# Kernel tuning notes

Measured on AMD Instinct MI355X. Metric: run time of the kernel, lower is better.

The kernel has to match this reference:

```python
import jax, jax.numpy as jnp
import numpy as np
from jax import lax

N_BOXES = 4000
NUM_CLASSES = 81  # class 0 is background, skipped like the torch loop


def _iou_matrix(boxes):
    # boxes: [N,4] as (x1,y1,x2,y2). Returns [N,N] pairwise IoU.
    x1, y1, x2, y2 = boxes[:, 0], boxes[:, 1], boxes[:, 2], boxes[:, 3]
    area = (x2 - x1) * (y2 - y1)
    ix1 = jnp.maximum(x1[:, None], x1[None, :])
    iy1 = jnp.maximum(y1[:, None], y1[None, :])
    ix2 = jnp.minimum(x2[:, None], x2[None, :])
    iy2 = jnp.minimum(y2[:, None], y2[None, :])
    inter = jnp.clip(ix2 - ix1, 0.0) * jnp.clip(iy2 - iy1, 0.0)
    return inter / (area[:, None] + area[None, :] - inter + 1e-9)


def _nms_keep(iou, score, valid, nms_thresh):
    # Greedy NMS in descending-score order, fixed shape. iou: [N,N].
    n = score.shape[0]
    order = jnp.argsort(-score)
    idx_range = jnp.arange(n)

    def body(i, keep):
        idx = order[i]
        cur = keep[idx]  # still alive -> it suppresses overlapping boxes
        row = iou[idx]
        sup = cur & (row > nms_thresh) & (idx_range != idx)
        return keep & ~sup

    keep = lax.fori_loop(0, n, body, valid)
    return keep & valid


def reference(bboxes, scores, conf_thresh, nms_thresh, max_instances):
    n = bboxes.shape[0]
    iou = _iou_matrix(bboxes)                       # [N,N], shared across classes
    scores_fg = scores[:, 1:].T                     # [C-1, N]
    valid = scores_fg > conf_thresh                 # per-class conf filter
    keep = jax.vmap(lambda s, v: _nms_keep(iou, s, v, nms_thresh))(scores_fg, valid)
    # Kept detections get their score; everything else -1 (padding sentinel).
    final = jnp.where(keep, scores_fg, -1.0)        # [C-1, N]
    top_vals, top_idx = lax.top_k(final.reshape(-1), max_instances)
    cls = top_idx // n                              # label = class_index - 1 (0-based fg)
    box_idx = top_idx % n
    preds = jnp.concatenate([bboxes[box_idx], top_vals[:, None]], axis=1)  # [K,5]
    valid_out = top_vals > 0.0
    preds = jnp.where(valid_out[:, None], preds, 0.0)
    labels = jnp.where(valid_out, cls, -1)
    return preds, labels


def setup_inputs() -> dict:
    key = jax.random.key(0)
    k1, k2, k3 = jax.random.split(key, 3)
    cxcy = jax.random.uniform(k1, (N_BOXES, 2), dtype=jnp.float32) * 1000.0
    wh = jax.random.uniform(k2, (N_BOXES, 2), dtype=jnp.float32) * 100.0 + 1.0
    bboxes = jnp.concatenate([cxcy - wh * 0.5, cxcy + wh * 0.5], axis=1)
    scores = jax.random.uniform(k3, (N_BOXES, NUM_CLASSES), dtype=jnp.float32)
    return {
        "bboxes": bboxes,
        "scores": scores,
        "conf_thresh": jnp.float32(0.5),
        "nms_thresh": jnp.float32(0.5),
        "max_instances": 100,
    }
```

## Files before the change

### kernel.cpp

```cpp
#include <hip/hip_runtime.h>
#include <stdint.h>

typedef unsigned long long u64;
typedef unsigned int u32;

#define NB    4000
#define NBP   4096
#define NCLS  80
#define ROWW  64
#define MAXI  100
#define NKEY  (NCLS * MAXI)
#define SMAX  4096
#define SELT  448
#define NTH   512

__device__ __forceinline__ u32 mono_f32(float f) {
    u32 u = __float_as_uint(f);
    return (u & 0x80000000u) ? ~u : (u | 0x80000000u);
}

__device__ __forceinline__ void find_cross(const u32* hist, int T, int lane,
                                           int* outB, int* outA) {
    int running = 0, B = -1, A = 0;
    for (int g = 0; g < 16 && B < 0; ++g) {
        const int d = 1023 - (g * 64 + lane);
        const int cnt = (int)hist[d];
        int pre = cnt;
        #pragma unroll
        for (int off = 1; off < 64; off <<= 1) {
            const int v = __shfl_up(pre, off);
            if (lane >= off) pre += v;
        }
        const int incl = running + pre;
        const int excl = incl - cnt;
        const u64 hm = __ballot(excl < T && incl >= T);
        if (hm != 0ull) {
            const int hl = (int)__builtin_ctzll(hm);
            B = __shfl(d, hl);
            A = __shfl(excl, hl);
        }
        running = __shfl(incl, 63);
    }
    *outB = B; *outA = A;
}

__global__ __launch_bounds__(256) void k_pre(const float4* __restrict__ boxes,
                                             const float* __restrict__ scores,
                                             const float* __restrict__ conf_t,
                                             const float* __restrict__ nms_t,
                                             u64* __restrict__ suppr,
                                             u64* __restrict__ pkeys) {
    const int tid = threadIdx.x;
    if (blockIdx.x < NB / 4) {
        const int i0  = blockIdx.x * 4;
        const float t = *nms_t;
        float4 bi[4]; float ai[4];
        #pragma unroll
        for (int r = 0; r < 4; ++r) {
            bi[r] = boxes[i0 + r];
            ai[r] = (bi[r].z - bi[r].x) * (bi[r].w - bi[r].y);
        }
        #pragma unroll
        for (int ch = 0; ch < 16; ++ch) {
            const int j = ch * 256 + tid;
            const bool inb = (j < NB);
            float4 bj = make_float4(0.f, 0.f, 0.f, 0.f);
            float aj = 0.f;
            if (inb) { bj = boxes[j]; aj = (bj.z - bj.x) * (bj.w - bj.y); }
            #pragma unroll
            for (int r = 0; r < 4; ++r) {
                bool bit = false;
                if (inb && j != i0 + r) {
                    const float ix1 = fmaxf(bi[r].x, bj.x), iy1 = fmaxf(bi[r].y, bj.y);
                    const float ix2 = fminf(bi[r].z, bj.z), iy2 = fminf(bi[r].w, bj.w);
                    const float inter = fmaxf(ix2 - ix1, 0.0f) * fmaxf(iy2 - iy1, 0.0f);
                    bit = inter / (ai[r] + aj - inter + 1e-9f) > t;
                }
                const u64 m = __ballot(bit);
                if ((tid & 63) == 0) suppr[(size_t)(i0 + r) * ROWW + (j >> 6)] = m;
            }
        }
    } else {
        const int idx = blockIdx.x - NB / 4;
        const int c   = idx >> 4;
        const int b   = ((idx & 15) << 8) | tid;
        const float conf = *conf_t;
        u64 key = 0;
        if (b < NB) {
            const float s = scores[b * 81 + c + 1];
            if (s > conf)
                key = ((u64)mono_f32(s) << 32) | (u64)(0xFFFFFFFFu - (u32)b);
        }
        pkeys[c * NBP + b] = key;
    }
}

__global__ __launch_bounds__(NTH) void k_classnms(const u64* __restrict__ pkeys,
                                                  const u64* __restrict__ suppr,
                                                  u64* __restrict__ cand) {
    __shared__ u64 skey[SMAX];
    __shared__ unsigned short sbox[SMAX];
    __shared__ int wsum[8];
    __shared__ int sh_kept, sh_M, sh_B, sh_A, sh_B2, sh_nvalid;

    u32* hist = (u32*)sbox;

    const int c    = blockIdx.x;
    const int tid  = threadIdx.x;
    const int lane = tid & 63;
    const int wid  = tid >> 6;

    u64 own[8];
    int cnt = 0;
    #pragma unroll
    for (int q = 0; q < 8; ++q) {
        own[q] = pkeys[c * NBP + tid + q * NTH];
        cnt += (own[q] != 0ull);
    }
    #pragma unroll
    for (int off = 1; off < 64; off <<= 1) cnt += __shfl_xor(cnt, off);
    if (lane == 0) wsum[wid] = cnt;
    __syncthreads();
    if (tid == 0) {
        int t = 0;
        #pragma unroll
        for (int w = 0; w < 8; ++w) t += wsum[w];
        sh_nvalid = t;
    }
    __syncthreads();
    const int nvalid = sh_nvalid;

    bool full = (nvalid <= 512);
    int kept = 0;

    for (int attempt = 0; attempt < 2; ++attempt) {
        int M;
        if (!full) {
            for (int i = tid; i < 1024; i += NTH) hist[i] = 0;
            if (tid == 0) sh_M = 0;
            __syncthreads();
            #pragma unroll
            for (int q = 0; q < 8; ++q)
                if (own[q] != 0ull)
                    atomicAdd(&hist[(u32)(own[q] >> 54) & 1023u], 1u);
            __syncthreads();
            if (tid < 64) {
                int B, A;
                find_cross(hist, SELT, lane, &B, &A);
                if (lane == 0) { sh_B = B; sh_A = A; }
            }
            __syncthreads();
            const int B = sh_B, A = sh_A;
            for (int i = tid; i < 1024; i += NTH) hist[i] = 0;
            __syncthreads();
            #pragma unroll
            for (int q = 0; q < 8; ++q)
                if (own[q] != 0ull && ((u32)(own[q] >> 54) & 1023u) == (u32)B)
                    atomicAdd(&hist[(u32)(own[q] >> 44) & 1023u], 1u);
            __syncthreads();
            if (tid < 64) {
                int B2, A2;
                find_cross(hist, SELT - A, lane, &B2, &A2);
                if (lane == 0) sh_B2 = B2;
            }
            __syncthreads();
            const int B2 = sh_B2;
            #pragma unroll
            for (int q = 0; q < 8; ++q) {
                bool sel = false;
                if (own[q] != 0ull) {
                    const int d = (int)((u32)(own[q] >> 54) & 1023u);
                    sel = (d > B) ||
                          (d == B && (int)((u32)(own[q] >> 44) & 1023u) >= B2);
                }
                const u64 bm = __ballot(sel);
                int wbase = 0;
                if (lane == 0 && bm) wbase = atomicAdd(&sh_M, (int)__popcll(bm));
                wbase = __shfl(wbase, 0);
                if (sel)
                    skey[wbase + (int)__popcll(bm & ((1ull << lane) - 1ull))] = own[q];
            }
            __syncthreads();
            M = sh_M;
        } else {
            if (tid == 0) sh_M = 0;
            __syncthreads();
            #pragma unroll
            for (int q = 0; q < 8; ++q) {
                const bool sel = (own[q] != 0ull);
                const u64 bm = __ballot(sel);
                int wbase = 0;
                if (lane == 0 && bm) wbase = atomicAdd(&sh_M, (int)__popcll(bm));
                wbase = __shfl(wbase, 0);
                if (sel)
                    skey[wbase + (int)__popcll(bm & ((1ull << lane) - 1ull))] = own[q];
            }
            __syncthreads();
            M = sh_M;
        }

        int S = 64;
        while (S < M) S <<= 1;
        for (int i = M + tid; i < S; i += NTH) skey[i] = 0;
        __syncthreads();

        for (int k2 = 2; k2 <= S; k2 <<= 1) {
            for (int j = k2 >> 1; j >= 64; j >>= 1) {
                for (int p = tid; p < (S >> 1); p += NTH) {
                    const int i0 = ((p & ~(j - 1)) << 1) | (p & (j - 1));
                    const u64 a = skey[i0], b = skey[i0 | j];
                    const bool up = ((i0 & k2) == 0);
                    if (up ? (a < b) : (a > b)) { skey[i0] = b; skey[i0 | j] = a; }
                }
                __syncthreads();
            }
            for (int base = 0; base < S; base += NTH) {
                const int i = base + tid;
                if (i < S) {
                    u64 x = skey[i];
                    #pragma unroll
                    for (int j2 = 32; j2 >= 1; j2 >>= 1) {
                        if (j2 < k2) {
                            const u64 y = __shfl_xor(x, j2);
                            const bool wantmax = (((i & k2) == 0) == ((i & j2) == 0));
                            x = wantmax ? (x > y ? x : y) : (x < y ? x : y);
                        }
                    }
                    skey[i] = x;
                }
            }
            __syncthreads();
        }

        for (int i = tid; i < S; i += NTH)
            sbox[i] = (unsigned short)(0xFFFFFFFFu - (u32)skey[i]);
        __syncthreads();

        if (tid < 64) {
            u64 keptmask = 0;
            int kp = 0;
            if (M > 0) {
                const int last = M - 1;
                u64 wA[16], wB[16];
                #pragma unroll
                for (int q = 0; q < 16; ++q) {
                    const int idx = (q <= last) ? q : last;
                    wA[q] = suppr[(size_t)sbox[idx] * ROWW + lane];
                }
                for (int cs = 0; cs < M && kp < MAXI; cs += 32) {
                    #pragma unroll
                    for (int q = 0; q < 16; ++q) {
                        const int want = cs + 16 + q;
                        const int idx = (want <= last) ? want : last;
                        wB[q] = suppr[(size_t)sbox[idx] * ROWW + lane];
                    }
                    #pragma unroll
                    for (int q = 0; q < 16; ++q) {
                        const int p = cs + q;
                        if (p < M && kp < MAXI) {
                            const bool sup = (__ballot((wA[q] & keptmask) != 0ull) != 0ull);
                            if (!sup) {
                                const int b = sbox[p];
                                if (lane == (b >> 6)) keptmask |= (1ull << (b & 63));
                                if (lane == 0) {
                                    const u32 mono = (u32)(skey[p] >> 32);
                                    const u32 flat = (u32)(c * NB + b);
                                    cand[c * MAXI + kp] =
                                        ((u64)mono << 32) | (u64)(0xFFFFFFFFu - flat);
                                }
                                kp++;
                            }
                        }
                    }
                    #pragma unroll
                    for (int q = 0; q < 16; ++q) {
                        const int want = cs + 32 + q;
                        const int idx = (want <= last) ? want : last;
                        wA[q] = suppr[(size_t)sbox[idx] * ROWW + lane];
                    }
                    #pragma unroll
                    for (int q = 0; q < 16; ++q) {
                        const int p = cs + 16 + q;
                        if (p < M && kp < MAXI) {
                            const bool sup = (__ballot((wB[q] & keptmask) != 0ull) != 0ull);
                            if (!sup) {
                                const int b = sbox[p];
                                if (lane == (b >> 6)) keptmask |= (1ull << (b & 63));
                                if (lane == 0) {
                                    const u32 mono = (u32)(skey[p] >> 32);
                                    const u32 flat = (u32)(c * NB + b);
                                    cand[c * MAXI + kp] =
                                        ((u64)mono << 32) | (u64)(0xFFFFFFFFu - flat);
                                }
                                kp++;
                            }
                        }
                    }
                }
            }
            if (lane == 0) sh_kept = kp;
        }
        __syncthreads();
        kept = sh_kept;

        if (kept >= MAXI || full) break;
        full = true;
    }

    for (int s = tid; s < MAXI; s += NTH)
        if (s >= kept) cand[c * MAXI + s] = 0;
}

__global__ __launch_bounds__(1024) void k_final(const u64* __restrict__ cand,
                                                const float4* __restrict__ boxes,
                                                float* __restrict__ out) {
    __shared__ u32 hist[1024];
    __shared__ u64 sel[256];
    __shared__ int wsum[16];
    __shared__ int sh_total, sh_A, sh_B, sh_bits, sh_M, sh_cnt;
    __shared__ u64 sh_prefix;

    const int tid  = threadIdx.x;
    const int lane = tid & 63;
    const int wid  = tid >> 6;

    u64 myk[8];
    int cnt = 0;
    #pragma unroll
    for (int q = 0; q < 8; ++q) {
        const int i = tid + (q << 10);
        myk[q] = (i < NKEY) ? cand[i] : 0ull;
        cnt += (myk[q] != 0ull);
    }
    #pragma unroll
    for (int off = 1; off < 64; off <<= 1) cnt += __shfl_xor(cnt, off);
    if (lane == 0) wsum[wid] = cnt;
    if (tid < 256) sel[tid] = 0;
    __syncthreads();
    if (tid == 0) {
        int t = 0;
        #pragma unroll
        for (int w = 0; w < 16; ++w) t += wsum[w];
        sh_total = t; sh_A = 0; sh_bits = 0; sh_prefix = 0; sh_cnt = 0;
    }
    __syncthreads();
    const int total = sh_total;
    const int Tt = (total < MAXI) ? total : MAXI;

    if (total > 0) {
        for (int lvl = 0; lvl < 6; ++lvl) {
            hist[tid & 1023] = 0;
            __syncthreads();
            const int bits = sh_bits;
            const u64 pref = sh_prefix;
            const int shift = 54 - bits;
            #pragma unroll
            for (int q = 0; q < 8; ++q) {
                const u64 k = myk[q];
                if (k != 0ull && (bits == 0 || (k >> (64 - bits)) == pref))
                    atomicAdd(&hist[(u32)(k >> shift) & 1023u], 1u);
            }
            __syncthreads();
            if (tid < 64) {
                const int T = Tt - sh_A;
                int B, A;
                find_cross(hist, T, lane, &B, &A);
                if (lane == 0) { sh_B = B; sh_A += A; }
            }
            __syncthreads();
            if (tid == 0) {
                sh_M = sh_A + (int)hist[sh_B];
                sh_prefix = (sh_prefix << 10) | (u32)sh_B;
                sh_bits += 10;
            }
            __syncthreads();
            if (sh_M <= 256) break;
        }
        const int bits = sh_bits;
        const u64 pref = sh_prefix;
        #pragma unroll
        for (int q = 0; q < 8; ++q) {
            const u64 k = myk[q];
            const bool s = (k != 0ull) && ((k >> (64 - bits)) >= pref);
            const u64 bm = __ballot(s);
            int wbase = 0;
            if (lane == 0 && bm) wbase = atomicAdd(&sh_cnt, (int)__popcll(bm));
            wbase = __shfl(wbase, 0);
            if (s) sel[wbase + (int)__popcll(bm & ((1ull << lane) - 1ull))] = k;
        }
    }

    if (tid < MAXI) {
        out[tid*5+0] = 0.0f; out[tid*5+1] = 0.0f; out[tid*5+2] = 0.0f;
        out[tid*5+3] = 0.0f; out[tid*5+4] = 0.0f;
        out[500 + tid] = -1.0f;
    }
    __syncthreads();
    if (tid < 256) {
        const u64 my = sel[tid];
        if (my != 0ull) {
            int r = 0;
            for (int j = 0; j < 256; ++j) r += (sel[j] > my);
            if (r < MAXI) {
                const u32 mono = (u32)(my >> 32);
                const float sc = __uint_as_float(mono ^ 0x80000000u);
                const u32 flat = 0xFFFFFFFFu - (u32)my;
                const int b    = (int)(flat % NB);
                const float4 bb = boxes[b];
                out[r*5+0] = bb.x; out[r*5+1] = bb.y;
                out[r*5+2] = bb.z; out[r*5+3] = bb.w;
                out[r*5+4] = sc;
                out[500 + r] = (float)(flat / NB);
            }
        }
    }
}

extern "C" void kernel_launch(void* const* d_in, const int* in_sizes, int n_in,
                              void* d_out, int out_size, void* d_ws, size_t ws_size,
                              hipStream_t stream) {
    const float4* bboxes = (const float4*)d_in[0];
    const float*  scores = (const float*)d_in[1];
    const float*  conf_t = (const float*)d_in[2];
    const float*  nms_t  = (const float*)d_in[3];

    char* ws = (char*)d_ws;
    u64* suppr = (u64*)ws;
    u64* pkeys = (u64*)(ws + 2048000);
    u64* cand  = (u64*)(ws + 2048000 + 2621440);

    k_pre<<<NB / 4 + 16 * NCLS, 256, 0, stream>>>(bboxes, scores, conf_t, nms_t,
                                                  suppr, pkeys);
    k_classnms<<<NCLS, NTH, 0, stream>>>(pkeys, suppr, cand);
    k_final<<<1, 1024, 0, stream>>>(cand, bboxes, (float*)d_out);
}
```

Before: 124.3 us.

## Replace precomputed IoU bitmask with on-the-fly IoU against kept boxes

Removes the kernel that built the full 4000x4000 suppression bitmask and the per-class key buffer. Each class block now builds its keys from scores directly and copies all boxes into shared memory. During the greedy scan it tests each candidate's IoU only against the at most 100 boxes already kept, held two per lane, instead of reading bitmask rows from global memory. This drops a launch and about 2 MB of global traffic, but the candidate loop becomes serial with a per-candidate division and shared-memory read and no prefetch batching.

```diff
diff --git a/kernel.cpp b/kernel.cpp
--- a/kernel.cpp
+++ b/kernel.cpp
@@ -5,9 +5,7 @@
 typedef unsigned int u32;
 
 #define NB    4000
-#define NBP   4096
 #define NCLS  80
-#define ROWW  64
 #define MAXI  100
 #define NKEY  (NCLS * MAXI)
 #define SMAX  4096
@@ -44,88 +42,49 @@
     *outB = B; *outA = A;
 }
 
-__global__ __launch_bounds__(256) void k_pre(const float4* __restrict__ boxes,
+__global__ __launch_bounds__(NTH) void k_nms(const float4* __restrict__ boxes,
                                              const float* __restrict__ scores,
                                              const float* __restrict__ conf_t,
                                              const float* __restrict__ nms_t,
-                                             u64* __restrict__ suppr,
-                                             u64* __restrict__ pkeys) {
-    const int tid = threadIdx.x;
-    if (blockIdx.x < NB / 4) {
-        const int i0  = blockIdx.x * 4;
-        const float t = *nms_t;
-        float4 bi[4]; float ai[4];
-        #pragma unroll
-        for (int r = 0; r < 4; ++r) {
-            bi[r] = boxes[i0 + r];
-            ai[r] = (bi[r].z - bi[r].x) * (bi[r].w - bi[r].y);
-        }
-        #pragma unroll
-        for (int ch = 0; ch < 16; ++ch) {
-            const int j = ch * 256 + tid;
-            const bool inb = (j < NB);
-            float4 bj = make_float4(0.f, 0.f, 0.f, 0.f);
-            float aj = 0.f;
-            if (inb) { bj = boxes[j]; aj = (bj.z - bj.x) * (bj.w - bj.y); }
-            #pragma unroll
-            for (int r = 0; r < 4; ++r) {
-                bool bit = false;
-                if (inb && j != i0 + r) {
-                    const float ix1 = fmaxf(bi[r].x, bj.x), iy1 = fmaxf(bi[r].y, bj.y);
-                    const float ix2 = fminf(bi[r].z, bj.z), iy2 = fminf(bi[r].w, bj.w);
-                    const float inter = fmaxf(ix2 - ix1, 0.0f) * fmaxf(iy2 - iy1, 0.0f);
-                    bit = inter / (ai[r] + aj - inter + 1e-9f) > t;
-                }
-                const u64 m = __ballot(bit);
-                if ((tid & 63) == 0) suppr[(size_t)(i0 + r) * ROWW + (j >> 6)] = m;
-            }
-        }
-    } else {
-        const int idx = blockIdx.x - NB / 4;
-        const int c   = idx >> 4;
-        const int b   = ((idx & 15) << 8) | tid;
-        const float conf = *conf_t;
-        u64 key = 0;
-        if (b < NB) {
-            const float s = scores[b * 81 + c + 1];
-            if (s > conf)
-                key = ((u64)mono_f32(s) << 32) | (u64)(0xFFFFFFFFu - (u32)b);
-        }
-        pkeys[c * NBP + b] = key;
-    }
-}
-
-__global__ __launch_bounds__(NTH) void k_classnms(const u64* __restrict__ pkeys,
-                                                  const u64* __restrict__ suppr,
-                                                  u64* __restrict__ cand) {
+                                             u64* __restrict__ cand) {
     __shared__ u64 skey[SMAX];
-    __shared__ unsigned short sbox[SMAX];
+    __shared__ float4 sboxes[NB];
+    __shared__ u32 hist[1024];
     __shared__ int wsum[8];
     __shared__ int sh_kept, sh_M, sh_B, sh_A, sh_B2, sh_nvalid;
-
-    u32* hist = (u32*)sbox;
 
     const int c    = blockIdx.x;
     const int tid  = threadIdx.x;
     const int lane = tid & 63;
     const int wid  = tid >> 6;
+    const float conf = *conf_t;
+    const float t    = *nms_t;
+
+    for (int i = tid; i < NB; i += NTH) sboxes[i] = boxes[i];
 
     u64 own[8];
     int cnt = 0;
     #pragma unroll
     for (int q = 0; q < 8; ++q) {
-        own[q] = pkeys[c * NBP + tid + q * NTH];
-        cnt += (own[q] != 0ull);
+        const int b = tid + q * NTH;
+        u64 k = 0;
+        if (b < NB) {
+            const float s = scores[b * 81 + c + 1];
+            if (s > conf)
+                k = ((u64)mono_f32(s) << 32) | (u64)(0xFFFFFFFFu - (u32)b);
+        }
+        own[q] = k;
+        cnt += (k != 0ull);
     }
     #pragma unroll
     for (int off = 1; off < 64; off <<= 1) cnt += __shfl_xor(cnt, off);
     if (lane == 0) wsum[wid] = cnt;
     __syncthreads();
     if (tid == 0) {
-        int t = 0;
+        int tt = 0;
         #pragma unroll
-        for (int w = 0; w < 8; ++w) t += wsum[w];
-        sh_nvalid = t;
+        for (int w = 0; w < 8; ++w) tt += wsum[w];
+        sh_nvalid = tt;
     }
     __syncthreads();
     const int nvalid = sh_nvalid;
@@ -232,69 +191,46 @@
             __syncthreads();
         }
 
-        for (int i = tid; i < S; i += NTH)
-            sbox[i] = (unsigned short)(0xFFFFFFFFu - (u32)skey[i]);
-        __syncthreads();
-
         if (tid < 64) {
-            u64 keptmask = 0;
+            float4 kb0 = make_float4(0.f,0.f,0.f,0.f), kb1 = kb0;
+            float ka0 = 0.f, ka1 = 0.f;
             int kp = 0;
             if (M > 0) {
-                const int last = M - 1;
-                u64 wA[16], wB[16];
-                #pragma unroll
-                for (int q = 0; q < 16; ++q) {
-                    const int idx = (q <= last) ? q : last;
-                    wA[q] = suppr[(size_t)sbox[idx] * ROWW + lane];
-                }
-                for (int cs = 0; cs < M && kp < MAXI; cs += 32) {
-                    #pragma unroll
-                    for (int q = 0; q < 16; ++q) {
-                        const int want = cs + 16 + q;
-                        const int idx = (want <= last) ? want : last;
-                        wB[q] = suppr[(size_t)sbox[idx] * ROWW + lane];
+                u64 kcur = skey[0];
+                float4 cbn = sboxes[0xFFFFFFFFu - (u32)kcur];
+                u64 knext = (M > 1) ? skey[1] : 0ull;
+                for (int p = 0; p < M && kp < MAXI; ++p) {
+                    const u64 kk = kcur;
+                    const float4 cb = cbn;
+                    if (p + 1 < M) cbn = sboxes[0xFFFFFFFFu - (u32)knext];
+                    kcur = knext;
+                    if (p + 2 < M) knext = skey[p + 2];
+                    const float ca = (cb.z - cb.x) * (cb.w - cb.y);
+                    bool sup;
+                    {
+                        const float ix1 = fmaxf(cb.x, kb0.x), iy1 = fmaxf(cb.y, kb0.y);
+                        const float ix2 = fminf(cb.z, kb0.z), iy2 = fminf(cb.w, kb0.w);
+                        const float inter = fmaxf(ix2 - ix1, 0.f) * fmaxf(iy2 - iy1, 0.f);
+                        sup = (lane < kp) && (inter / (ka0 + ca - inter + 1e-9f) > t);
                     }
-                    #pragma unroll
-                    for (int q = 0; q < 16; ++q) {
-                        const int p = cs + q;
-                        if (p < M && kp < MAXI) {
-                            const bool sup = (__ballot((wA[q] & keptmask) != 0ull) != 0ull);
-                            if (!sup) {
-                                const int b = sbox[p];
-                                if (lane == (b >> 6)) keptmask |= (1ull << (b & 63));
-                                if (lane == 0) {
-                                    const u32 mono = (u32)(skey[p] >> 32);
-                                    const u32 flat = (u32)(c * NB + b);
-                                    cand[c * MAXI + kp] =
-                                        ((u64)mono << 32) | (u64)(0xFFFFFFFFu - flat);
-                                }
-                                kp++;
-                            }
+                    {
+                        const float ix1 = fmaxf(cb.x, kb1.x), iy1 = fmaxf(cb.y, kb1.y);
+                        const float ix2 = fminf(cb.z, kb1.z), iy2 = fminf(cb.w, kb1.w);
+                        const float inter = fmaxf(ix2 - ix1, 0.f) * fmaxf(iy2 - iy1, 0.f);
+                        sup |= (64 + lane < kp) && (inter / (ka1 + ca - inter + 1e-9f) > t);
+                    }
+                    if (__ballot(sup) == 0ull) {
+                        if (lane == (kp & 63)) {
+                            if (kp < 64) { kb0 = cb; ka0 = ca; }
+                            else         { kb1 = cb; ka1 = ca; }
                         }
-                    }
-                    #pragma unroll
-                    for (int q = 0; q < 16; ++q) {
-                        const int want = cs + 32 + q;
-                        const int idx = (want <= last) ? want : last;
-                        wA[q] = suppr[(size_t)sbox[idx] * ROWW + lane];
-                    }
-                    #pragma unroll
-                    for (int q = 0; q < 16; ++q) {
-                        const int p = cs + 16 + q;
-                        if (p < M && kp < MAXI) {
-                            const bool sup = (__ballot((wB[q] & keptmask) != 0ull) != 0ull);
-                            if (!sup) {
-                                const int b = sbox[p];
-                                if (lane == (b >> 6)) keptmask |= (1ull << (b & 63));
-                                if (lane == 0) {
-                                    const u32 mono = (u32)(skey[p] >> 32);
-                                    const u32 flat = (u32)(c * NB + b);
-                                    cand[c * MAXI + kp] =
-                                        ((u64)mono << 32) | (u64)(0xFFFFFFFFu - flat);
-                                }
-                                kp++;
-                            }
+                        if (lane == 0) {
+                            const u32 b = 0xFFFFFFFFu - (u32)kk;
+                            const u32 flat = (u32)(c * NB + (int)b);
+                            cand[c * MAXI + kp] =
+                                (kk & 0xFFFFFFFF00000000ull) | (u64)(0xFFFFFFFFu - flat);
                         }
+                        kp++;
                     }
                 }
             }
@@ -424,13 +360,8 @@
     const float*  conf_t = (const float*)d_in[2];
     const float*  nms_t  = (const float*)d_in[3];
 
-    char* ws = (char*)d_ws;
-    u64* suppr = (u64*)ws;
-    u64* pkeys = (u64*)(ws + 2048000);
-    u64* cand  = (u64*)(ws + 2048000 + 2621440);
-
-    k_pre<<<NB / 4 + 16 * NCLS, 256, 0, stream>>>(bboxes, scores, conf_t, nms_t,
-                                                  suppr, pkeys);
-    k_classnms<<<NCLS, NTH, 0, stream>>>(pkeys, suppr, cand);
+    u64* cand = (u64*)d_ws;
+
+    k_nms<<<NCLS, NTH, 0, stream>>>(bboxes, scores, conf_t, nms_t, cand);
     k_final<<<1, 1024, 0, stream>>>(cand, bboxes, (float*)d_out);
 }
```

Result: slower. 127.2 us (+2.3%).
